# Kernel optimization log

Hardware: AMD Instinct MI355X
Metric: run time of the kernel (lower is better)

Reference implementation:

```python
import jax, jax.numpy as jnp
import numpy as np

V, H, E, L = 50257, 1024, 512, 128


def setup_inputs() -> dict:
    key = jax.random.key(0)
    ks = jax.random.split(key, 16)
    s = 0.02
    return {
        "input_tok": jax.random.randint(ks[0], (1,), 0, V),
        "h0": jax.random.normal(ks[1], (1, 1, H), jnp.float32),
        "c0": jax.random.normal(ks[2], (1, 1, H), jnp.float32),
        "enc_output": jax.random.normal(ks[3], (L, H), jnp.float32),
        "emb_table": s * jax.random.normal(ks[4], (V, E), jnp.float32),
        "attn_W": s * jax.random.normal(ks[5], (L, H + E), jnp.float32),
        "attn_b": jnp.zeros((L,), jnp.float32),
        "a2d_W": s * jax.random.normal(ks[6], (H, H + E), jnp.float32),
        "a2d_b": jnp.zeros((H,), jnp.float32),
        "W_ih": s * jax.random.normal(ks[7], (4 * H, H), jnp.float32),
        "W_hh": s * jax.random.normal(ks[8], (4 * H, H), jnp.float32),
        "b_ih": jnp.zeros((4 * H,), jnp.float32),
        "b_hh": jnp.zeros((4 * H,), jnp.float32),
        "out_W": s * jax.random.normal(ks[9], (V, H), jnp.float32),
        "out_b": jnp.zeros((V,), jnp.float32),
    }


def reference(input_tok, h0, c0, enc_output, emb_table, attn_W, attn_b,
              a2d_W, a2d_b, W_ih, W_hh, b_ih, b_hh, out_W, out_b):
    # embed: (1, E); h, c: (1, H)
    embed = emb_table[input_tok].reshape(1, E)
    h = h0.reshape(1, H)
    c = c0.reshape(1, H)
    # attention over encoder positions
    attn_in = jnp.concatenate([embed, h], axis=1)                      # (1, E+H)
    attn_weight = jax.nn.softmax(attn_in @ attn_W.T + attn_b, axis=1)  # (1, L)
    attn_out = attn_weight @ enc_output                                # (1, H)
    # combine and project to LSTM input
    dec_in = jnp.concatenate([embed, attn_out], axis=1)                # (1, E+H)
    dec_in = jax.nn.relu(dec_in @ a2d_W.T + a2d_b)                     # (1, H)
    # one LSTM cell step (torch gate order: i, f, g, o)
    gates = dec_in @ W_ih.T + b_ih + h @ W_hh.T + b_hh                 # (1, 4H)
    i_g, f_g, g_g, o_g = jnp.split(gates, 4, axis=1)
    c_new = jax.nn.sigmoid(f_g) * c + jax.nn.sigmoid(i_g) * jnp.tanh(g_g)
    h_new = jax.nn.sigmoid(o_g) * jnp.tanh(c_new)
    # output log-probs over vocab
    output = jax.nn.log_softmax(h_new @ out_W.T + out_b, axis=1)       # (1, V)
    return output, h_new.reshape(1, 1, H), c_new.reshape(1, 1, H), attn_weight
```

## Files before the change

### kernel.cpp

```cpp
#include <hip/hip_runtime.h>
#include <math.h>

#define V 50257
#define H 1024
#define E 512
#define L 128
#define HE 1536
#define NBLK5 2048
#define VSTRIDE (NBLK5 * 4)

#define WS_DECRAW 0
#define WS_DECIN  1536
#define WS_HNEW   2560
#define WS_GHH    3584
#define WS_ALOGIT 7680
#define WS_PAIRS  7808

__device__ __forceinline__ float wave_reduce_sum(float v) {
    #pragma unroll
    for (int off = 32; off > 0; off >>= 1) v += __shfl_xor(v, off, 64);
    return v;
}

__global__ __launch_bounds__(256)
void k_attn_whh(const int* __restrict__ tok_p,
                const float* __restrict__ h0,
                const float* __restrict__ emb,
                const float* __restrict__ attn_W,
                const float* __restrict__ attn_b,
                const float* __restrict__ W_hh,
                float* __restrict__ ws) {
    const int tid = threadIdx.x, lane = tid & 63, w = tid >> 6;
    const int bid = blockIdx.x;

    if (bid >= 128) {
        const int j = bid - 128;
        const float4* h4 = (const float4*)h0;
        const float4* wh4 = (const float4*)(W_hh + ((size_t)w * H + j) * H);
        float acc = 0.f;
        #pragma unroll
        for (int k = 0; k < 4; ++k) {
            float4 b = wh4[lane + (k << 6)];
            float4 h = h4[lane + (k << 6)];
            acc = fmaf(b.x, h.x, acc); acc = fmaf(b.y, h.y, acc);
            acc = fmaf(b.z, h.z, acc); acc = fmaf(b.w, h.w, acc);
        }
        acc = wave_reduce_sum(acc);
        if (lane == 0) ws[WS_GHH + w * H + j] = acc;
        return;
    }

    __shared__ float s_in[HE];
    __shared__ float s_part[4];
    const int tok = tok_p[0];
    for (int k = tid; k < HE; k += 256) {
        float v = (k < E) ? emb[(size_t)tok * E + k] : h0[k - E];
        s_in[k] = v;
        if (bid == 0 && k < E) ws[WS_DECRAW + k] = v;
    }
    __syncthreads();
    const float* wr = attn_W + (size_t)bid * HE;
    float acc = 0.f;
    #pragma unroll
    for (int i = 0; i < 6; ++i)
        acc = fmaf(s_in[tid + (i << 8)], wr[tid + (i << 8)], acc);
    acc = wave_reduce_sum(acc);
    if (lane == 0) s_part[w] = acc;
    __syncthreads();
    if (tid == 0)
        ws[WS_ALOGIT + bid] = s_part[0] + s_part[1] + s_part[2] + s_part[3]
                              + attn_b[bid];
}

__global__ void k_attn_out(const float* __restrict__ enc,
                           float* __restrict__ out_attnw,
                           float* __restrict__ ws) {
    __shared__ float s_wn[L];
    __shared__ float s_acc[4][64];
    const int tid = threadIdx.x;
    if (tid < L) s_wn[tid] = ws[WS_ALOGIT + tid];
    __syncthreads();
    float m = -1e30f;
    #pragma unroll
    for (int l = 0; l < L; ++l) m = fmaxf(m, s_wn[l]);
    float s = 0.f;
    #pragma unroll
    for (int l = 0; l < L; ++l) s += __expf(s_wn[l] - m);
    __syncthreads();
    if (tid < L) {
        float wn = __expf(s_wn[tid] - m) / s;
        s_wn[tid] = wn;
        if (blockIdx.x == 0) out_attnw[tid] = wn;
    }
    __syncthreads();
    const int j = blockIdx.x * 64 + (tid & 63);
    const int lg = tid >> 6;
    float acc = 0.f;
    #pragma unroll
    for (int li = 0; li < 32; ++li) {
        const int l = (lg << 5) + li;
        acc = fmaf(s_wn[l], enc[l * H + j], acc);
    }
    s_acc[lg][tid & 63] = acc;
    __syncthreads();
    if (tid < 64) {
        float r = s_acc[0][tid] + s_acc[1][tid] + s_acc[2][tid] + s_acc[3][tid];
        ws[WS_DECRAW + E + blockIdx.x * 64 + tid] = r;
    }
}

__global__ void k_a2d(const float* __restrict__ a2d_W,
                      const float* __restrict__ a2d_b,
                      float* __restrict__ ws) {
    __shared__ float s_part[6];
    const int tid = threadIdx.x, lane = tid & 63, w = tid >> 6;
    const int r = blockIdx.x;
    const float4* x4 = (const float4*)(ws + WS_DECRAW);
    const float4* w4 = (const float4*)(a2d_W + (size_t)r * HE);
    float4 a = x4[lane + (w << 6)];
    float4 b = w4[lane + (w << 6)];
    float acc = a.x * b.x + a.y * b.y + a.z * b.z + a.w * b.w;
    acc = wave_reduce_sum(acc);
    if (lane == 0) s_part[w] = acc;
    __syncthreads();
    if (tid == 0) {
        float t = s_part[0] + s_part[1] + s_part[2] + s_part[3] + s_part[4] + s_part[5];
        ws[WS_DECIN + r] = fmaxf(t + a2d_b[r], 0.f);
    }
}

__global__ void k_lstm(const float* __restrict__ c0,
                       const float* __restrict__ W_ih,
                       const float* __restrict__ b_ih,
                       const float* __restrict__ b_hh,
                       float* __restrict__ out_h,
                       float* __restrict__ out_c,
                       float* __restrict__ ws) {
    __shared__ float s_g[4];
    const int tid = threadIdx.x, lane = tid & 63, w = tid >> 6;
    const int j = blockIdx.x;
    const float4* x4 = (const float4*)(ws + WS_DECIN);
    const float4* wi4 = (const float4*)(W_ih + ((size_t)w * H + j) * H);
    float acc = 0.f;
    #pragma unroll
    for (int k = 0; k < 4; ++k) {
        float4 a = wi4[lane + (k << 6)];
        float4 x = x4[lane + (k << 6)];
        acc = fmaf(a.x, x.x, acc); acc = fmaf(a.y, x.y, acc);
        acc = fmaf(a.z, x.z, acc); acc = fmaf(a.w, x.w, acc);
    }
    acc = wave_reduce_sum(acc);
    if (lane == 0) s_g[w] = acc + ws[WS_GHH + w * H + j];
    __syncthreads();
    if (tid == 0) {
        float gi_ = s_g[0] + b_ih[j]         + b_hh[j];
        float gf  = s_g[1] + b_ih[H + j]     + b_hh[H + j];
        float gg  = s_g[2] + b_ih[2 * H + j] + b_hh[2 * H + j];
        float go  = s_g[3] + b_ih[3 * H + j] + b_hh[3 * H + j];
        float si = 1.f / (1.f + expf(-gi_));
        float sf = 1.f / (1.f + expf(-gf));
        float so = 1.f / (1.f + expf(-go));
        float cn = sf * c0[j] + si * tanhf(gg);
        float hn = so * tanhf(cn);
        out_c[j] = cn;
        out_h[j] = hn;
        ws[WS_HNEW + j] = hn;
    }
}

__global__ void k_vocab(const float* __restrict__ out_W,
                        const float* __restrict__ out_b,
                        float* __restrict__ logits,
                        float* __restrict__ ws) {
    const int lane = threadIdx.x & 63;
    const int widx = threadIdx.x >> 6;
    const int gw = (blockIdx.x << 2) + widx;
    const float4* h4 = (const float4*)(ws + WS_HNEW);
    float4 hr[4];
    #pragma unroll
    for (int k = 0; k < 4; ++k) hr[k] = h4[lane + (k << 6)];
    float m = -1e30f, s = 0.f;
    for (int v = gw; v < V; v += 2 * VSTRIDE) {
        const int v2 = v + VSTRIDE;
        const float4* w0 = (const float4*)(out_W + (size_t)v * H);
        float acc0 = 0.f, acc1 = 0.f;
        #pragma unroll
        for (int k = 0; k < 4; ++k) {
            float4 a = w0[lane + (k << 6)];
            acc0 = fmaf(hr[k].x, a.x, acc0); acc0 = fmaf(hr[k].y, a.y, acc0);
            acc0 = fmaf(hr[k].z, a.z, acc0); acc0 = fmaf(hr[k].w, a.w, acc0);
        }
        if (v2 < V) {
            const float4* w1 = (const float4*)(out_W + (size_t)v2 * H);
            #pragma unroll
            for (int k = 0; k < 4; ++k) {
                float4 a = w1[lane + (k << 6)];
                acc1 = fmaf(hr[k].x, a.x, acc1); acc1 = fmaf(hr[k].y, a.y, acc1);
                acc1 = fmaf(hr[k].z, a.z, acc1); acc1 = fmaf(hr[k].w, a.w, acc1);
            }
        }
        acc0 = wave_reduce_sum(acc0);
        float l0 = acc0 + out_b[v];
        if (lane == 0) logits[v] = l0;
        float mo = m;
        m = fmaxf(m, l0);
        s = s * __expf(mo - m) + __expf(l0 - m);
        if (v2 < V) {
            acc1 = wave_reduce_sum(acc1);
            float l1 = acc1 + out_b[v2];
            if (lane == 0) logits[v2] = l1;
            mo = m;
            m = fmaxf(m, l1);
            s = s * __expf(mo - m) + __expf(l1 - m);
        }
    }
    __shared__ float sm[4], ss[4];
    if (lane == 0) { sm[widx] = m; ss[widx] = s; }
    __syncthreads();
    if (threadIdx.x == 0) {
        float M = sm[0], S = ss[0];
        #pragma unroll
        for (int i = 1; i < 4; ++i) {
            float Mn = fmaxf(M, sm[i]);
            S = S * __expf(M - Mn) + ss[i] * __expf(sm[i] - Mn);
            M = Mn;
        }
        ws[WS_PAIRS + 2 * blockIdx.x]     = M;
        ws[WS_PAIRS + 2 * blockIdx.x + 1] = S;
    }
}

__global__ void k_final(float* __restrict__ logits,
                        const float* __restrict__ ws) {
    __shared__ float sm[256], ss[256];
    const int tid = threadIdx.x;
    float M = -1e30f, S = 0.f;
    for (int i = tid; i < NBLK5; i += 256) {
        float m2 = ws[WS_PAIRS + 2 * i], s2 = ws[WS_PAIRS + 2 * i + 1];
        float Mn = fmaxf(M, m2);
        S = S * __expf(M - Mn) + s2 * __expf(m2 - Mn);
        M = Mn;
    }
    sm[tid] = M; ss[tid] = S;
    __syncthreads();
    for (int off = 128; off > 0; off >>= 1) {
        if (tid < off) {
            float m2 = sm[tid + off], s2 = ss[tid + off];
            float Mn = fmaxf(sm[tid], m2);
            ss[tid] = ss[tid] * __expf(sm[tid] - Mn) + s2 * __expf(m2 - Mn);
            sm[tid] = Mn;
        }
        __syncthreads();
    }
    const float C = sm[0] + logf(ss[0]);
    for (int v = blockIdx.x * 256 + tid; v < V; v += gridDim.x * 256)
        logits[v] -= C;
}

extern "C" void kernel_launch(void* const* d_in, const int* in_sizes, int n_in,
                              void* d_out, int out_size, void* d_ws, size_t ws_size,
                              hipStream_t stream) {
    const int*   tok    = (const int*)d_in[0];
    const float* h0     = (const float*)d_in[1];
    const float* c0     = (const float*)d_in[2];
    const float* enc    = (const float*)d_in[3];
    const float* emb    = (const float*)d_in[4];
    const float* attn_W = (const float*)d_in[5];
    const float* attn_b = (const float*)d_in[6];
    const float* a2d_W  = (const float*)d_in[7];
    const float* a2d_b  = (const float*)d_in[8];
    const float* W_ih   = (const float*)d_in[9];
    const float* W_hh   = (const float*)d_in[10];
    const float* b_ih   = (const float*)d_in[11];
    const float* b_hh   = (const float*)d_in[12];
    const float* out_W  = (const float*)d_in[13];
    const float* out_b  = (const float*)d_in[14];

    float* out        = (float*)d_out;
    float* ws         = (float*)d_ws;
    float* out_logits = out;
    float* out_h      = out + V;
    float* out_c      = out + V + H;
    float* out_attnw  = out + V + 2 * H;

    k_attn_whh<<<1152, 256, 0, stream>>>(tok, h0, emb, attn_W, attn_b, W_hh, ws);
    k_attn_out<<<16, 256, 0, stream>>>(enc, out_attnw, ws);
    k_a2d<<<1024, 384, 0, stream>>>(a2d_W, a2d_b, ws);
    k_lstm<<<1024, 256, 0, stream>>>(c0, W_ih, b_ih, b_hh, out_h, out_c, ws);
    k_vocab<<<NBLK5, 256, 0, stream>>>(out_W, out_b, out_logits, ws);
    k_final<<<256, 256, 0, stream>>>(out_logits, ws);
}
```

Before: 65.66 us.

## Fully unroll vocab GEMV rows with double-buffered register prefetch

Replaces the strided loop over vocabulary rows in the vocab projection kernel with a fixed, fully unrolled sequence of seven rows per wave. Loads for the next pair of rows are issued into a second register buffer before the current pair is reduced, so more memory requests stay in flight. This assumes V fits within 7*NWAVE5 rows, which holds for V=50257. It adds register pressure from the 16 float4 buffers, which could lower occupancy.

```diff
diff --git a/kernel.cpp b/kernel.cpp
--- a/kernel.cpp
+++ b/kernel.cpp
@@ -7,7 +7,7 @@
 #define L 128
 #define HE 1536
 #define NBLK5 2048
-#define VSTRIDE (NBLK5 * 4)
+#define NWAVE5 (NBLK5 * 4)
 
 #define WS_DECRAW 0
 #define WS_DECIN  1536
@@ -179,41 +179,83 @@
     float4 hr[4];
     #pragma unroll
     for (int k = 0; k < 4; ++k) hr[k] = h4[lane + (k << 6)];
+
+    const int v6 = gw + 6 * NWAVE5;
+    const bool valid6 = (v6 < V);
+    const int v6c = valid6 ? v6 : (V - 1);
+
+    float4 A[8], B[8];
     float m = -1e30f, s = 0.f;
-    for (int v = gw; v < V; v += 2 * VSTRIDE) {
-        const int v2 = v + VSTRIDE;
-        const float4* w0 = (const float4*)(out_W + (size_t)v * H);
-        float acc0 = 0.f, acc1 = 0.f;
+    float lg[7];
+
+    #define LOAD2(dst, va, vb)                                                \
+        {                                                                     \
+            const float4* p0 = (const float4*)(out_W + (size_t)(va) * H);     \
+            const float4* p1 = (const float4*)(out_W + (size_t)(vb) * H);     \
+            _Pragma("unroll")                                                 \
+            for (int k = 0; k < 4; ++k) {                                     \
+                dst[k]     = p0[lane + (k << 6)];                             \
+                dst[4 + k] = p1[lane + (k << 6)];                             \
+            }                                                                 \
+        }
+    #define RED2(src, i0, i1)                                                 \
+        {                                                                     \
+            float t0 = 0.f, t1 = 0.f;                                         \
+            _Pragma("unroll")                                                 \
+            for (int k = 0; k < 4; ++k) {                                     \
+                t0 = fmaf(src[k].x, hr[k].x, t0);                             \
+                t0 = fmaf(src[k].y, hr[k].y, t0);                             \
+                t0 = fmaf(src[k].z, hr[k].z, t0);                             \
+                t0 = fmaf(src[k].w, hr[k].w, t0);                             \
+                t1 = fmaf(src[4 + k].x, hr[k].x, t1);                         \
+                t1 = fmaf(src[4 + k].y, hr[k].y, t1);                         \
+                t1 = fmaf(src[4 + k].z, hr[k].z, t1);                         \
+                t1 = fmaf(src[4 + k].w, hr[k].w, t1);                         \
+            }                                                                 \
+            t0 = wave_reduce_sum(t0);                                         \
+            t1 = wave_reduce_sum(t1);                                         \
+            lg[i0] = t0 + out_b[gw + (i0) * NWAVE5];                          \
+            lg[i1] = t1 + out_b[gw + (i1) * NWAVE5];                          \
+            float mo = m;                                                     \
+            m = fmaxf(m, fmaxf(lg[i0], lg[i1]));                              \
+            s = s * __expf(mo - m) + __expf(lg[i0] - m) + __expf(lg[i1] - m); \
+        }
+
+    LOAD2(A, gw, gw + NWAVE5);
+    LOAD2(B, gw + 2 * NWAVE5, gw + 3 * NWAVE5);
+    RED2(A, 0, 1);
+    LOAD2(A, gw + 4 * NWAVE5, gw + 5 * NWAVE5);
+    RED2(B, 2, 3);
+    {
+        const float4* p0 = (const float4*)(out_W + (size_t)v6c * H);
+        #pragma unroll
+        for (int k = 0; k < 4; ++k) B[k] = p0[lane + (k << 6)];
+    }
+    RED2(A, 4, 5);
+    {
+        float t0 = 0.f;
         #pragma unroll
         for (int k = 0; k < 4; ++k) {
-            float4 a = w0[lane + (k << 6)];
-            acc0 = fmaf(hr[k].x, a.x, acc0); acc0 = fmaf(hr[k].y, a.y, acc0);
-            acc0 = fmaf(hr[k].z, a.z, acc0); acc0 = fmaf(hr[k].w, a.w, acc0);
-        }
-        if (v2 < V) {
-            const float4* w1 = (const float4*)(out_W + (size_t)v2 * H);
-            #pragma unroll
-            for (int k = 0; k < 4; ++k) {
-                float4 a = w1[lane + (k << 6)];
-                acc1 = fmaf(hr[k].x, a.x, acc1); acc1 = fmaf(hr[k].y, a.y, acc1);
-                acc1 = fmaf(hr[k].z, a.z, acc1); acc1 = fmaf(hr[k].w, a.w, acc1);
-            }
-        }
-        acc0 = wave_reduce_sum(acc0);
-        float l0 = acc0 + out_b[v];
-        if (lane == 0) logits[v] = l0;
-        float mo = m;
-        m = fmaxf(m, l0);
-        s = s * __expf(mo - m) + __expf(l0 - m);
-        if (v2 < V) {
-            acc1 = wave_reduce_sum(acc1);
-            float l1 = acc1 + out_b[v2];
-            if (lane == 0) logits[v2] = l1;
-            mo = m;
-            m = fmaxf(m, l1);
-            s = s * __expf(mo - m) + __expf(l1 - m);
-        }
-    }
+            t0 = fmaf(B[k].x, hr[k].x, t0); t0 = fmaf(B[k].y, hr[k].y, t0);
+            t0 = fmaf(B[k].z, hr[k].z, t0); t0 = fmaf(B[k].w, hr[k].w, t0);
+        }
+        t0 = wave_reduce_sum(t0);
+        lg[6] = t0 + out_b[v6c];
+        if (valid6) {
+            float mo = m;
+            m = fmaxf(m, lg[6]);
+            s = s * __expf(mo - m) + __expf(lg[6] - m);
+        }
+    }
+    #undef LOAD2
+    #undef RED2
+
+    if (lane == 0) {
+        #pragma unroll
+        for (int i = 0; i < 6; ++i) logits[gw + i * NWAVE5] = lg[i];
+        if (valid6) logits[v6] = lg[6];
+    }
+
     __shared__ float sm[4], ss[4];
     if (lane == 0) { sm[widx] = m; ss[widx] = s; }
     __syncthreads();
```

Result: faster. 64.30 us (-2.1%).
